# Kernel optimization log

Measured on AMD Instinct MI355X. Metric: run time of the kernel, lower is better.

The kernel has to match this reference:

```python
import jax, jax.numpy as jnp
import numpy as np

B, T, D = 256, 256, 96   # batch, seq (== block_size), d_model
H, E = 6, 16             # n_head, d_head = d_model // n_head
DFF = 4 * D              # feedforward hidden = 384
NOISE_STD = 0.1
EPS = 1e-5               # torch LayerNorm default eps


def setup_inputs() -> dict:
    key = jax.random.key(0)
    ks = jax.random.split(key, 10)
    s = 0.02
    return {
        "x":     jax.random.normal(ks[0], (B, T, D), jnp.float32),
        # per-head Q/K/V projections stacked: [H, D, E] (no bias, as in Head)
        "Wq":    jax.random.normal(ks[1], (H, D, E), jnp.float32) * s,
        "Wk":    jax.random.normal(ks[2], (H, D, E), jnp.float32) * s,
        "Wv":    jax.random.normal(ks[3], (H, D, E), jnp.float32) * s,
        "Wp":    jax.random.normal(ks[4], (D, D), jnp.float32) * s,
        "bp":    jnp.zeros((D,), jnp.float32),
        "ln1_g": jnp.ones((D,), jnp.float32),
        "ln1_b": jnp.zeros((D,), jnp.float32),
        "ln2_g": jnp.ones((D,), jnp.float32),
        "ln2_b": jnp.zeros((D,), jnp.float32),
        "W1":    jax.random.normal(ks[5], (D, DFF), jnp.float32) * s,
        "b1":    jnp.zeros((DFF,), jnp.float32),
        "W2":    jax.random.normal(ks[6], (DFF, D), jnp.float32) * s,
        "b2":    jnp.zeros((D,), jnp.float32),
    }


def layernorm(x, g, b):
    m = jnp.mean(x, axis=-1, keepdims=True)
    v = jnp.var(x, axis=-1, keepdims=True)
    return (x - m) * jax.lax.rsqrt(v + EPS) * g + b


def reference(x, Wq, Wk, Wv, Wp, bp, ln1_g, ln1_b, ln2_g, ln2_b, W1, b1, W2, b2):
    Bx, Tx, Dx = x.shape
    nk1, nk2 = jax.random.split(jax.random.key(42), 2)

    # --- self-attention branch (pre-norm) ---
    h = layernorm(x, ln1_g, ln1_b)
    q = jnp.einsum('btd,hde->bhte', h, Wq)
    k = jnp.einsum('btd,hde->bhte', h, Wk)
    v = jnp.einsum('btd,hde->bhte', h, Wv)
    scores = jnp.einsum('bhte,bhse->bhts', q, k) * (E ** -0.5)
    causal = jnp.tril(jnp.ones((Tx, Tx), bool))
    scores = jnp.where(causal, scores, -jnp.inf)
    a = jax.nn.softmax(scores, axis=-1)      # dropout = identity (eval)
    o = jnp.einsum('bhts,bhse->bhte', a, v)
    o = o.transpose(0, 2, 1, 3).reshape(Bx, Tx, Dx)  # concat heads
    o = o @ Wp + bp
    x = x + o + jax.random.normal(nk1, x.shape, x.dtype) * NOISE_STD

    # --- feedforward branch (pre-norm) ---
    h = layernorm(x, ln2_g, ln2_b)
    f = jax.nn.relu(h @ W1 + b1) @ W2 + b2   # dropout = identity (eval)
    x = x + f + jax.random.normal(nk2, x.shape, x.dtype) * NOISE_STD
    return x
```

## Files before the change

### kernel.cpp

```cpp
#include <hip/hip_runtime.h>
#include <hip/hip_bf16.h>
#include <stdint.h>


#define B_    256
#define T_    256
#define D_    96
#define H_    6
#define E_    16
#define DFF_  384
#define BT_   (B_*T_)
#define NTOK_ (BT_*D_)
#define WPN_  (96*96)
#define W1N_  (96*384)
#define W2N_  (384*96)
#define WTOT_ (WPN_+W1N_+W2N_)

typedef __hip_bfloat16 bf16;
typedef __attribute__((ext_vector_type(8))) short v8s;
typedef __attribute__((ext_vector_type(4))) short v4s;
typedef __attribute__((ext_vector_type(4))) float v4f;

__device__ __forceinline__ void wfence(){ __asm__ volatile("" ::: "memory"); }

__host__ __device__ inline uint32_t rotl32(uint32_t x, int r){ return (x<<r)|(x>>(32-r)); }

__host__ __device__ inline void tf2x32(uint32_t k0, uint32_t k1, uint32_t& x0, uint32_t& x1){
  uint32_t ks2 = k0 ^ k1 ^ 0x1BD11BDAu;
  x0 += k0; x1 += k1;
#define TF_R(r) { x0 += x1; x1 = rotl32(x1, r); x1 ^= x0; }
  TF_R(13) TF_R(15) TF_R(26) TF_R(6)
  x0 += k1;  x1 += ks2 + 1u;
  TF_R(17) TF_R(29) TF_R(16) TF_R(24)
  x0 += ks2; x1 += k0 + 2u;
  TF_R(13) TF_R(15) TF_R(26) TF_R(6)
  x0 += k0;  x1 += k1 + 3u;
  TF_R(17) TF_R(29) TF_R(16) TF_R(24)
  x0 += k1;  x1 += ks2 + 4u;
  TF_R(13) TF_R(15) TF_R(26) TF_R(6)
  x0 += ks2; x1 += k0 + 5u;
#undef TF_R
}

__device__ __forceinline__ float erfinv32(float x){
  float w = -0.69314718056f * __log2f((1.0f - x) * (1.0f + x));
  float p;
  if (w < 5.0f) {
    w -= 2.5f;
    p = 2.81022636e-08f;
    p = fmaf(p, w, 3.43273939e-07f);
    p = fmaf(p, w, -3.5233877e-06f);
    p = fmaf(p, w, -4.39150654e-06f);
    p = fmaf(p, w, 0.00021858087f);
    p = fmaf(p, w, -0.00125372503f);
    p = fmaf(p, w, -0.00417768164f);
    p = fmaf(p, w, 0.246640727f);
    p = fmaf(p, w, 1.50140941f);
  } else {
    w = sqrtf(w) - 3.0f;
    p = -0.000200214257f;
    p = fmaf(p, w, 0.000100950558f);
    p = fmaf(p, w, 0.00134934322f);
    p = fmaf(p, w, -0.00367342844f);
    p = fmaf(p, w, 0.00573950773f);
    p = fmaf(p, w, -0.0076224613f);
    p = fmaf(p, w, 0.00943887047f);
    p = fmaf(p, w, 1.00167406f);
    p = fmaf(p, w, 2.83297682f);
  }
  return p * x;
}

__device__ __forceinline__ float jax_normal(uint32_t k0, uint32_t k1, uint32_t j){
  uint32_t x0 = 0u, x1 = j;
  tf2x32(k0, k1, x0, x1);
  uint32_t bits = x0 ^ x1;
  float f = __uint_as_float((bits >> 9) | 0x3F800000u) - 1.0f;
  const float lo = -0.99999994f;
  float u = fmaxf(lo, fmaf(f, 2.0f, lo));
  return 1.41421356f * erfinv32(u);
}

__device__ __forceinline__ float blo(uint32_t u){ return __uint_as_float(u << 16); }
__device__ __forceinline__ float bhi(uint32_t u){ return __uint_as_float(u & 0xFFFF0000u); }
__device__ __forceinline__ uint16_t f2b(float f){
  union { bf16 h; uint16_t u; } x; x.h = __float2bfloat16(f); return x.u;
}
__device__ __forceinline__ uint32_t packbf(float a, float b){
  return (uint32_t)f2b(a) | ((uint32_t)f2b(b) << 16);
}
__device__ __forceinline__ v4s pack4(float a, float b, float c, float d){
  uint64_t both = ((uint64_t)packbf(c, d) << 32) | (uint64_t)packbf(a, b);
  v4s r; __builtin_memcpy(&r, &both, 8); return r;
}

__device__ __forceinline__ v4f mfma16(v4s a, v4s b, v4f c){
#if __has_builtin(__builtin_amdgcn_mfma_f32_16x16x16_bf16)
  return __builtin_amdgcn_mfma_f32_16x16x16_bf16(a, b, c, 0, 0, 0);
#elif __has_builtin(__builtin_amdgcn_mfma_f32_16x16x16bf16_1k)
  return __builtin_amdgcn_mfma_f32_16x16x16bf16_1k(a, b, c, 0, 0, 0);
#else
  v4f d;
  asm volatile("v_mfma_f32_16x16x16_bf16 %0, %1, %2, %3"
               : "=v"(d) : "v"(a), "v"(b), "v"(c));
  return d;
#endif
}

__global__ __launch_bounds__(256, 4)
void k_attn_fused(const float* __restrict__ x,
                  const float* __restrict__ Wq, const float* __restrict__ Wk,
                  const float* __restrict__ Wv,
                  const float* __restrict__ g1, const float* __restrict__ bln1,
                  bf16* __restrict__ o_ws,
                  const float* __restrict__ Wp, const float* __restrict__ W1,
                  const float* __restrict__ W2, bf16* __restrict__ wbuf)
{
  __shared__ __align__(16) uint16_t hts[64*104];
  __shared__ __align__(16) uint32_t wpl[48][52];
  __shared__ __align__(16) uint16_t Ks[256][16];
  __shared__ __align__(16) uint16_t Vt[16][264];

  const int tid  = threadIdx.x;
  const int bh   = blockIdx.x;
  const int b    = bh / H_, h = bh % H_;
  const int w    = tid >> 6;
  const int lane = tid & 63;
  const int quad = lane >> 4;
  const int l15  = lane & 15;

  if (tid < 54) {
    int id = bh*54 + tid;
    const float* src; bf16* dst; int k, n, N;
    if (id < WPN_)             { src = Wp; dst = wbuf;               k = id/96; n = id%96; N = 96; }
    else if (id < WPN_ + W1N_) { int t = id - WPN_;
                                 src = W1; dst = wbuf + WPN_;        k = t/384; n = t%384; N = 384; }
    else                       { int t = id - WPN_ - W1N_;
                                 src = W2; dst = wbuf + WPN_ + W1N_; k = t/96;  n = t%96;  N = 96; }
    int idx = ((k>>3)*(N>>4) + (n>>4))*128 + ((n&15)<<3) + (k&7);
    dst[idx] = __float2bfloat16(src[(size_t)k*N + n]);
  }

  for (int idx = tid; idx < 48*48; idx += 256) {
    int c = idx / 48, dp = idx % 48;
    int mat = c >> 4, e = c & 15;
    const float* Wm = (mat == 0 ? Wk : (mat == 1 ? Wv : Wq)) + h*(D_*E_);
    wpl[c][dp] = packbf(Wm[(2*dp)*16 + e], Wm[(2*dp+1)*16 + e]);
  }
  __syncthreads();

  v4f qacc[4];
  {
    const int r  = lane >> 2;
    const int cg = lane & 3;
    float gv[24], bv[24];
    #pragma unroll
    for (int i = 0; i < 24; ++i) { gv[i] = g1[cg*24 + i]; bv[i] = bln1[cg*24 + i]; }

    for (int rt = 0; rt < 4; ++rt) {
      wfence();
      const int lrow = w*16 + r;
      const int row  = rt*64 + lrow;
      const float4* xp = (const float4*)(x + ((size_t)(b*256 + row)*96 + cg*24));
      float xv[24];
      #pragma unroll
      for (int p = 0; p < 6; ++p) {
        float4 t4 = xp[p];
        xv[4*p+0] = t4.x; xv[4*p+1] = t4.y; xv[4*p+2] = t4.z; xv[4*p+3] = t4.w;
      }
      float s1 = 0.f, s2 = 0.f;
      #pragma unroll
      for (int i = 0; i < 24; ++i) { s1 += xv[i]; s2 = fmaf(xv[i], xv[i], s2); }
      s1 += __shfl_xor(s1, 1); s2 += __shfl_xor(s2, 1);
      s1 += __shfl_xor(s1, 2); s2 += __shfl_xor(s2, 2);
      float mm = s1 * (1.0f/96.0f);
      float rs = rsqrtf(s2 * (1.0f/96.0f) - mm*mm + 1e-5f);
      #pragma unroll
      for (int p = 0; p < 12; ++p) {
        float h0 = (xv[2*p]   - mm)*rs*gv[2*p]   + bv[2*p];
        float h1 = (xv[2*p+1] - mm)*rs*gv[2*p+1] + bv[2*p+1];
        *(uint32_t*)&hts[lrow*104 + cg*24 + 2*p] = packbf(h0, h1);
      }
      wfence();

      v8s ah[3];
      #pragma unroll
      for (int ks = 0; ks < 3; ++ks)
        ah[ks] = *(const v8s*)&hts[(w*16 + l15)*104 + ks*32 + quad*8];
      #pragma unroll
      for (int nt = 0; nt < 3; ++nt) {
        v4f acc = {0.f,0.f,0.f,0.f};
        #pragma unroll
        for (int ks = 0; ks < 3; ++ks) {
          v8s bb = *(const v8s*)&wpl[nt*16 + l15][ks*16 + quad*4];
          acc = __builtin_amdgcn_mfma_f32_16x16x32_bf16(ah[ks], bb, acc, 0, 0, 0);
        }
        int tr0 = rt*64 + w*16 + quad*4;
        if (nt == 0) {
          #pragma unroll
          for (int r2 = 0; r2 < 4; ++r2) Ks[tr0 + r2][l15] = f2b(acc[r2]);
        } else if (nt == 1) {
          *(uint32_t*)&Vt[l15][tr0]     = packbf(acc[0], acc[1]);
          *(uint32_t*)&Vt[l15][tr0 + 2] = packbf(acc[2], acc[3]);
        } else {
          qacc[rt] = acc;
        }
      }
    }
  }
  __syncthreads();

  uint16_t* Pb = &hts[(w*16)*104];
  v8s qf[4];
  v8s zero8;
  #pragma unroll
  for (int j = 0; j < 8; ++j) zero8[j] = 0;
  #pragma unroll
  for (int rt = 0; rt < 4; ++rt) {
    wfence();
    #pragma unroll
    for (int r2 = 0; r2 < 4; ++r2)
      Pb[(quad*4 + r2)*40 + l15] = f2b(qacc[rt][r2] * 0.25f);
    wfence();
    qf[rt] = (quad < 2) ? *(const v8s*)&Pb[l15*40 + quad*8] : zero8;
  }

  v4s ones4;
  #pragma unroll
  for (int j = 0; j < 4; ++j) ones4[j] = (short)0x3F80;

  v4f oacc[4], lac[4];
  #pragma unroll
  for (int i = 0; i < 4; ++i) { oacc[i] = (v4f){0.f,0.f,0.f,0.f}; lac[i] = (v4f){0.f,0.f,0.f,0.f}; }

  for (int sb = 0; sb < 8; ++sb) {
    v8s kf0 = (quad < 2) ? *(const v8s*)&Ks[sb*32      + l15][quad*8] : zero8;
    v8s kf1 = (quad < 2) ? *(const v8s*)&Ks[sb*32 + 16 + l15][quad*8] : zero8;
    v4s vb0 = *(const v4s*)&Vt[l15][sb*32      + quad*4];
    v4s vb1 = *(const v4s*)&Vt[l15][sb*32 + 16 + quad*4];
    const int sbase = sb*32 + quad*4;
    #pragma unroll
    for (int i = 0; i < 4; ++i) {
      int mt = 4*i + w;
      if (mt >= 2*sb) {
        v4f z = {0.f,0.f,0.f,0.f};
        v4f s0t = __builtin_amdgcn_mfma_f32_16x16x32_bf16(kf0, qf[i], z, 0, 0, 0);
        v4f s1t = __builtin_amdgcn_mfma_f32_16x16x32_bf16(kf1, qf[i], z, 0, 0, 0);
        const int qg = mt*16 + l15;
        float p00 = (sbase + 0      > qg) ? 0.f : __expf(s0t[0]);
        float p01 = (sbase + 1      > qg) ? 0.f : __expf(s0t[1]);
        float p02 = (sbase + 2      > qg) ? 0.f : __expf(s0t[2]);
        float p03 = (sbase + 3      > qg) ? 0.f : __expf(s0t[3]);
        float p10 = (sbase + 16     > qg) ? 0.f : __expf(s1t[0]);
        float p11 = (sbase + 17     > qg) ? 0.f : __expf(s1t[1]);
        float p12 = (sbase + 18     > qg) ? 0.f : __expf(s1t[2]);
        float p13 = (sbase + 19     > qg) ? 0.f : __expf(s1t[3]);
        v4s pa0 = pack4(p00, p01, p02, p03);
        v4s pa1 = pack4(p10, p11, p12, p13);
        oacc[i] = mfma16(pa0, vb0,   oacc[i]);
        oacc[i] = mfma16(pa1, vb1,   oacc[i]);
        lac[i]  = mfma16(pa0, ones4, lac[i]);
        lac[i]  = mfma16(pa1, ones4, lac[i]);
      }
    }
  }

  #pragma unroll
  for (int i = 0; i < 4; ++i) {
    int mt = 4*i + w;
    #pragma unroll
    for (int r2 = 0; r2 < 4; ++r2) {
      float inv = 1.0f / lac[i][r2];
      size_t idx = ((size_t)b*256 + mt*16 + quad*4 + r2)*96 + h*16 + l15;
      o_ws[idx] = __float2bfloat16(oacc[i][r2] * inv);
    }
  }
}

__global__ __launch_bounds__(256, 8)
void k_proj_ff(const float* __restrict__ x, const bf16* __restrict__ o_ws,
               const bf16* __restrict__ wb,
               const float* __restrict__ bp,
               const float* __restrict__ g2, const float* __restrict__ bln2,
               const float* __restrict__ b1, const float* __restrict__ b2,
               float* __restrict__ out,
               uint32_t n1k0, uint32_t n1k1, uint32_t n2k0, uint32_t n2k1)
{
  __shared__ __align__(16) uint16_t t2[2][32][104];
  __shared__ __align__(8)  float2  st[32][2];

  const bf16* wpb = wb;
  const bf16* w1b = wb + WPN_;
  const bf16* w2b = wb + WPN_ + W1N_;

  const int tid  = threadIdx.x;
  const int w    = tid >> 6;
  const int wp   = w >> 1;
  const int s    = w & 1;
  const int lane = tid & 63;
  const int quad = lane >> 4;
  const int l15  = lane & 15;
  const int rowbase = blockIdx.x * 32;
  const uint32_t jbase = (uint32_t)rowbase * 96u;
  const int rloc = wp*16 + quad*4;

  #define BFRAG(Wb, Ndiv16, nt, k8) \
    (*(const v8s*)((Wb) + (((k8)*(Ndiv16) + (nt))*128 + l15*8)))

  uint32_t ffp[6];
  {
    float ff[12];
    {
      v8s ao[3];
      #pragma unroll
      for (int ks = 0; ks < 3; ++ks)
        ao[ks] = *(const v8s*)(o_ws + (size_t)(rowbase + wp*16 + l15)*96 + ks*32 + quad*8);
      #pragma unroll
      for (int nt3 = 0; nt3 < 3; ++nt3) {
        int nt = s*3 + nt3;
        int col = nt*16 + l15;
        v4f acc = {0.f,0.f,0.f,0.f};
        #pragma unroll
        for (int ks = 0; ks < 3; ++ks)
          acc = __builtin_amdgcn_mfma_f32_16x16x32_bf16(ao[ks], BFRAG(wpb, 6, nt, ks*4+quad), acc, 0, 0, 0);
        float bpv = bp[col];
        #pragma unroll
        for (int r = 0; r < 4; ++r) {
          int row = rloc + r;
          uint32_t j = jbase + (uint32_t)row*96u + (uint32_t)col;
          ff[nt3*4+r] = acc[r] + bpv + x[j] + 0.1f * jax_normal(n1k0, n1k1, j);
        }
      }
    }

    float s1p[4], s2p[4];
    #pragma unroll
    for (int r = 0; r < 4; ++r) {
      float s1 = 0.f, s2 = 0.f;
      #pragma unroll
      for (int nt3 = 0; nt3 < 3; ++nt3) { float v = ff[nt3*4+r]; s1 += v; s2 = fmaf(v, v, s2); }
      s1 += __shfl_xor(s1, 1); s2 += __shfl_xor(s2, 1);
      s1 += __shfl_xor(s1, 2); s2 += __shfl_xor(s2, 2);
      s1 += __shfl_xor(s1, 4); s2 += __shfl_xor(s2, 4);
      s1 += __shfl_xor(s1, 8); s2 += __shfl_xor(s2, 8);
      s1p[r] = s1; s2p[r] = s2;
    }
    if (l15 == 0) {
      #pragma unroll
      for (int r = 0; r < 4; ++r) st[rloc + r][s] = make_float2(s1p[r], s2p[r]);
    }
    __syncthreads();

    float g2v[3], b2l[3];
    #pragma unroll
    for (int nt3 = 0; nt3 < 3; ++nt3) {
      g2v[nt3] = g2[s*48 + nt3*16 + l15];
      b2l[nt3] = bln2[s*48 + nt3*16 + l15];
    }
    #pragma unroll
    for (int r = 0; r < 4; ++r) {
      float2 pa = st[rloc + r][0], pb = st[rloc + r][1];
      float s1 = pa.x + pb.x, s2 = pa.y + pb.y;
      float mm = s1 * (1.0f/96.0f);
      float rs = rsqrtf(s2 * (1.0f/96.0f) - mm*mm + 1e-5f);
      #pragma unroll
      for (int nt3 = 0; nt3 < 3; ++nt3)
        t2[0][rloc + r][s*48 + nt3*16 + l15] =
            f2b((ff[nt3*4+r] - mm) * rs * g2v[nt3] + b2l[nt3]);
    }

    #pragma unroll
    for (int nt3 = 0; nt3 < 3; ++nt3) {
      ffp[nt3*2]   = packbf(ff[nt3*4+0], ff[nt3*4+1]);
      ffp[nt3*2+1] = packbf(ff[nt3*4+2], ff[nt3*4+3]);
    }
  }
  __syncthreads();

  v8s ah[3];
  #pragma unroll
  for (int ks = 0; ks < 3; ++ks)
    ah[ks] = *(const v8s*)&t2[0][wp*16 + l15][ks*32 + quad*8];
  v4f acc2[3];
  #pragma unroll
  for (int nt3 = 0; nt3 < 3; ++nt3) acc2[nt3] = (v4f){0.f,0.f,0.f,0.f};

  #define FF1C(C, DST) { \
    _Pragma("unroll") \
    for (int nt3 = 0; nt3 < 3; ++nt3) { \
      v4f a = {0.f,0.f,0.f,0.f}; \
      _Pragma("unroll") \
      for (int ks = 0; ks < 3; ++ks) \
        a = __builtin_amdgcn_mfma_f32_16x16x32_bf16(ah[ks], BFRAG(w1b, 24, (C)*6 + s*3 + nt3, ks*4+quad), a, 0, 0, 0); \
      float b1v = b1[(C)*96 + s*48 + nt3*16 + l15]; \
      _Pragma("unroll") \
      for (int r = 0; r < 4; ++r) \
        DST[rloc + r][s*48 + nt3*16 + l15] = f2b(fmaxf(a[r] + b1v, 0.f)); \
    } }

  #define FF2C(C, SRC) { \
    v8s af[3]; \
    _Pragma("unroll") \
    for (int ks = 0; ks < 3; ++ks) \
      af[ks] = *(const v8s*)&SRC[wp*16 + l15][ks*32 + quad*8]; \
    _Pragma("unroll") \
    for (int nt3 = 0; nt3 < 3; ++nt3) { \
      _Pragma("unroll") \
      for (int ks = 0; ks < 3; ++ks) \
        acc2[nt3] = __builtin_amdgcn_mfma_f32_16x16x32_bf16(af[ks], BFRAG(w2b, 6, s*3 + nt3, ((C)*3+ks)*4+quad), acc2[nt3], 0, 0, 0); \
    } }

  FF1C(0, t2[1])
  __syncthreads();
  FF1C(1, t2[0])
  FF2C(0, t2[1])
  __syncthreads();
  FF1C(2, t2[1])
  FF2C(1, t2[0])
  __syncthreads();
  FF1C(3, t2[0])
  FF2C(2, t2[1])
  __syncthreads();
  FF2C(3, t2[0])

  #pragma unroll
  for (int nt3 = 0; nt3 < 3; ++nt3) {
    int col = s*48 + nt3*16 + l15;
    float b2v = b2[col];
    #pragma unroll
    for (int r = 0; r < 4; ++r) {
      int row = rloc + r;
      uint32_t j = jbase + (uint32_t)row*96u + (uint32_t)col;
      uint32_t pk = ffp[nt3*2 + (r>>1)];
      float x1v = (r&1) ? bhi(pk) : blo(pk);
      out[(size_t)(rowbase + row)*96 + col] =
          x1v + acc2[nt3][r] + b2v + 0.1f * jax_normal(n2k0, n2k1, j);
    }
  }
  #undef FF2C
  #undef FF1C
  #undef BFRAG
}

__global__ __launch_bounds__(256)
void k_zero(float* __restrict__ out)
{
  int i = blockIdx.x*256 + threadIdx.x;
  if (i < NTOK_) out[i] = 0.0f;
}

extern "C" void kernel_launch(void* const* d_in, const int* in_sizes, int n_in,
                              void* d_out, int out_size, void* d_ws, size_t ws_size,
                              hipStream_t stream) {
  const float* x    = (const float*)d_in[0];
  const float* Wq   = (const float*)d_in[1];
  const float* Wk   = (const float*)d_in[2];
  const float* Wv   = (const float*)d_in[3];
  const float* Wp   = (const float*)d_in[4];
  const float* bp   = (const float*)d_in[5];
  const float* g1   = (const float*)d_in[6];
  const float* bln1 = (const float*)d_in[7];
  const float* g2   = (const float*)d_in[8];
  const float* bln2 = (const float*)d_in[9];
  const float* W1   = (const float*)d_in[10];
  const float* b1   = (const float*)d_in[11];
  const float* W2   = (const float*)d_in[12];
  const float* b2   = (const float*)d_in[13];
  float* out = (float*)d_out;

  size_t need = (size_t)NTOK_*sizeof(bf16) + (size_t)WTOT_*sizeof(bf16);
  if (ws_size < need) {
    hipLaunchKernelGGL(k_zero, dim3((NTOK_ + 255)/256), dim3(256), 0, stream, out);
    return;
  }
  bf16* o_ws = (bf16*)d_ws;
  bf16* wbuf = o_ws + NTOK_;

  uint32_t n1k0 = 0u, n1k1 = 0u; tf2x32(0u, 42u, n1k0, n1k1);
  uint32_t n2k0 = 0u, n2k1 = 1u; tf2x32(0u, 42u, n2k0, n2k1);

  hipLaunchKernelGGL(k_attn_fused, dim3(B_*H_), dim3(256), 0, stream,
                     x, Wq, Wk, Wv, g1, bln1, o_ws, Wp, W1, W2, wbuf);
  hipLaunchKernelGGL(k_proj_ff, dim3(BT_/32), dim3(256), 0, stream,
                     x, o_ws, wbuf, bp, g2, bln2, b1, b2, out,
                     n1k0, n1k1, n2k0, n2k1);
}
```

Before: 190.9 us.

## Replace double-buffered FF hidden tile with single buffer and reload LN2 rows per chunk

```diff
diff --git a/kernel.cpp b/kernel.cpp
--- a/kernel.cpp
+++ b/kernel.cpp
@@ -286,7 +286,8 @@
                float* __restrict__ out,
                uint32_t n1k0, uint32_t n1k1, uint32_t n2k0, uint32_t n2k1)
 {
-  __shared__ __align__(16) uint16_t t2[2][32][104];
+  __shared__ __align__(16) uint16_t t2h[32][104];
+  __shared__ __align__(16) uint16_t f1b[32][104];
   __shared__ __align__(8)  float2  st[32][2];
 
   const bf16* wpb = wb;
@@ -365,7 +366,7 @@
       float rs = rsqrtf(s2 * (1.0f/96.0f) - mm*mm + 1e-5f);
       #pragma unroll
       for (int nt3 = 0; nt3 < 3; ++nt3)
-        t2[0][rloc + r][s*48 + nt3*16 + l15] =
+        t2h[rloc + r][s*48 + nt3*16 + l15] =
             f2b((ff[nt3*4+r] - mm) * rs * g2v[nt3] + b2l[nt3]);
     }
 
@@ -377,32 +378,32 @@
   }
   __syncthreads();
 
-  v8s ah[3];
-  #pragma unroll
-  for (int ks = 0; ks < 3; ++ks)
-    ah[ks] = *(const v8s*)&t2[0][wp*16 + l15][ks*32 + quad*8];
   v4f acc2[3];
   #pragma unroll
   for (int nt3 = 0; nt3 < 3; ++nt3) acc2[nt3] = (v4f){0.f,0.f,0.f,0.f};
 
-  #define FF1C(C, DST) { \
+  #define FF1C(C) { \
+    v8s ahc[3]; \
+    _Pragma("unroll") \
+    for (int ks = 0; ks < 3; ++ks) \
+      ahc[ks] = *(const v8s*)&t2h[wp*16 + l15][ks*32 + quad*8]; \
     _Pragma("unroll") \
     for (int nt3 = 0; nt3 < 3; ++nt3) { \
       v4f a = {0.f,0.f,0.f,0.f}; \
       _Pragma("unroll") \
       for (int ks = 0; ks < 3; ++ks) \
-        a = __builtin_amdgcn_mfma_f32_16x16x32_bf16(ah[ks], BFRAG(w1b, 24, (C)*6 + s*3 + nt3, ks*4+quad), a, 0, 0, 0); \
+        a = __builtin_amdgcn_mfma_f32_16x16x32_bf16(ahc[ks], BFRAG(w1b, 24, (C)*6 + s*3 + nt3, ks*4+quad), a, 0, 0, 0); \
       float b1v = b1[(C)*96 + s*48 + nt3*16 + l15]; \
       _Pragma("unroll") \
       for (int r = 0; r < 4; ++r) \
-        DST[rloc + r][s*48 + nt3*16 + l15] = f2b(fmaxf(a[r] + b1v, 0.f)); \
+        f1b[rloc + r][s*48 + nt3*16 + l15] = f2b(fmaxf(a[r] + b1v, 0.f)); \
     } }
 
-  #define FF2C(C, SRC) { \
+  #define FF2C(C) { \
     v8s af[3]; \
     _Pragma("unroll") \
     for (int ks = 0; ks < 3; ++ks) \
-      af[ks] = *(const v8s*)&SRC[wp*16 + l15][ks*32 + quad*8]; \
+      af[ks] = *(const v8s*)&f1b[wp*16 + l15][ks*32 + quad*8]; \
     _Pragma("unroll") \
     for (int nt3 = 0; nt3 < 3; ++nt3) { \
       _Pragma("unroll") \
@@ -410,18 +411,21 @@
         acc2[nt3] = __builtin_amdgcn_mfma_f32_16x16x32_bf16(af[ks], BFRAG(w2b, 6, s*3 + nt3, ((C)*3+ks)*4+quad), acc2[nt3], 0, 0, 0); \
     } }
 
-  FF1C(0, t2[1])
-  __syncthreads();
-  FF1C(1, t2[0])
-  FF2C(0, t2[1])
-  __syncthreads();
-  FF1C(2, t2[1])
-  FF2C(1, t2[0])
-  __syncthreads();
-  FF1C(3, t2[0])
-  FF2C(2, t2[1])
-  __syncthreads();
-  FF2C(3, t2[0])
+  FF1C(0)
+  __syncthreads();
+  FF2C(0)
+  __syncthreads();
+  FF1C(1)
+  __syncthreads();
+  FF2C(1)
+  __syncthreads();
+  FF1C(2)
+  __syncthreads();
+  FF2C(2)
+  __syncthreads();
+  FF1C(3)
+  __syncthreads();
+  FF2C(3)
 
   #pragma unroll
   for (int nt3 = 0; nt3 < 3; ++nt3) {
```

New measurement: 193.7 us. Within noise of the previous version (+1.5%).
